# Optimization experiments

Measured on AMD Instinct MI355X. Metric: run time of the kernel, lower is better.

Reference implementation:

```python
import jax, jax.numpy as jnp
import numpy as np

T = 2048      # sequence length (single unbatched sequence)
V = 32000     # vocab
D = 1024      # d_model
E = 16        # number of experts (one structural group)
TOPK = 2      # router top-k
CAP = 256     # per-expert capacity (T*TOPK/E)
DFF = 2048    # expert MLP hidden
NHOPS = 2     # number of routing hops
EPS = 1e-5    # RMSNorm eps


def setup_inputs() -> dict:
    key = jax.random.key(0)
    ks = jax.random.split(key, 6)
    ids = jax.random.randint(ks[0], (T,), 0, V)
    embed_W = jax.random.normal(ks[1], (V, D), jnp.float32) * 0.02
    ln_scale = jnp.ones((D,), jnp.float32)
    router_W = jax.random.normal(ks[2], (NHOPS, D, E), jnp.float32) * (D ** -0.5)
    expert_W1 = jax.random.normal(ks[3], (NHOPS, E, D, DFF), jnp.float32) * (D ** -0.5)
    expert_W2 = jax.random.normal(ks[4], (NHOPS, E, DFF, D), jnp.float32) * (DFF ** -0.5)
    return dict(ids=ids, embed_W=embed_W, ln_scale=ln_scale,
                router_W=router_W, expert_W1=expert_W1, expert_W2=expert_W2)


def _hop(h, Wr, W1, W2):
    # Router: clean logits -> mixing probs (softmax) + hard top-k selection mask.
    logits = h @ Wr                                   # (T, E)
    probs = jax.nn.softmax(logits, axis=-1)           # (T, E)
    _, top = jax.lax.top_k(logits, TOPK)              # (T, TOPK)
    mask = jnp.zeros((T, E), bool).at[jnp.arange(T)[:, None], top].set(True)

    # _capacity_select: rank tokens per expert by clean logits, keep top CAP.
    m = mask.T                                        # (E, T)
    g = jnp.where(m, logits.T, -jnp.inf)              # (E, T)
    _, top_idx = jax.lax.top_k(g, CAP)                # (E, C)
    slot = jnp.zeros((E, CAP, T), h.dtype)
    slot = slot.at[jnp.arange(E)[:, None], jnp.arange(CAP)[None, :], top_idx].set(1.0)
    slot = slot * m[:, None, :].astype(h.dtype)       # zero slots filled from -inf
    kept = slot.sum(1) > 0                            # (E, T)

    # One-hot einsum gather of token states into expert slot buffers.
    xin = jnp.einsum('ect,td->ecd', slot, h)          # (E, C, D)

    # Stable sort slots by original token position (active slots first).
    active = slot.sum(-1) > 0                         # (E, C)
    pos = jnp.where(active, top_idx, T + 1)
    order = jnp.argsort(pos, axis=1, stable=True)     # (E, C)
    xin = jnp.take_along_axis(xin, order[:, :, None], axis=1)
    slot = jnp.take_along_axis(slot, order[:, :, None], axis=1)

    # Grouped (stacked/vmapped) expert execution: GELU MLP per expert.
    h1 = jax.nn.gelu(jnp.einsum('ecd,edf->ecf', xin, W1))
    expert_out = jnp.einsum('ecf,efd->ecd', h1, W2)   # (E, C, D)

    # Combine (Eq. 3): h_{s+1} = h_s + sum_e rho_e (M_e(h) - h)
    cw = jnp.where(kept.T, probs, 0.0)                # (T, E)
    rho = cw.sum(axis=1, keepdims=True)               # (T, 1)
    combine = jnp.einsum('ecd,ect,et->td', expert_out, slot, cw.T)
    return h + combine - rho * h


def reference(ids, embed_W, ln_scale, router_W, expert_W1, expert_W2):
    h = embed_W[ids]                                  # (T, D) embedding lookup
    for i in range(NHOPS):
        h = _hop(h, router_W[i], expert_W1[i], expert_W2[i])
    # RMSNorm + tied unembedding
    h = h * jax.lax.rsqrt(jnp.mean(h * h, axis=-1, keepdims=True) + EPS) * ln_scale
    return h @ embed_W.T                              # (T, V)
```

## Files before the change

### kernel.cpp

```cpp
#include <hip/hip_runtime.h>
#include <stdint.h>

#define T_ 2048
#define V_ 32000
#define D_ 1024
#define E_ 16
#define CAP_ 256
#define DFF_ 2048

typedef unsigned short u16;
typedef unsigned int u32;
typedef __bf16 bf16x8 __attribute__((ext_vector_type(8)));
typedef float f32x4 __attribute__((ext_vector_type(4)));

__device__ __forceinline__ u16 f2bf(float f){
  u32 u = __float_as_uint(f);
  u32 r = u + 0x7FFFu + ((u >> 16) & 1u);
  return (u16)(r >> 16);
}
__device__ __forceinline__ float bf2f(u16 s){ return __uint_as_float(((u32)s) << 16); }

__device__ __forceinline__ void gl_lds16(const void* g, void* l){
  __builtin_amdgcn_global_load_lds((const __attribute__((address_space(1))) void*)g,
                                   (__attribute__((address_space(3))) void*)l, 16, 0, 0);
}
__device__ __forceinline__ f32x4 mfma16(bf16x8 a, bf16x8 b, f32x4 c){
  return __builtin_amdgcn_mfma_f32_16x16x32_bf16(a, b, c, 0, 0, 0);
}
__device__ __forceinline__ float gelu_tanh(float x){
  float u = 0.7978845608028654f * (x + 0.044715f * x * x * x);
  return 0.5f * x * (1.0f + tanhf(u));
}

__global__ __launch_bounds__(256) void k_embed(const int* __restrict__ ids,
    const float* __restrict__ W, float* __restrict__ h){
  int t = blockIdx.x;
  int d = threadIdx.x * 4;
  *(float4*)(h + (size_t)t*D_ + d) = *(const float4*)(W + (size_t)ids[t]*D_ + d);
}

__global__ __launch_bounds__(256) void k_cvtw(const float* __restrict__ W, u16* __restrict__ Wb){
  size_t i = ((size_t)blockIdx.x*256 + threadIdx.x)*8;
  float4 a = *(const float4*)(W + i);
  float4 b = *(const float4*)(W + i + 4);
  union { u16 s[8]; uint4 v; } p;
  p.s[0]=f2bf(a.x); p.s[1]=f2bf(a.y); p.s[2]=f2bf(a.z); p.s[3]=f2bf(a.w);
  p.s[4]=f2bf(b.x); p.s[5]=f2bf(b.y); p.s[6]=f2bf(b.z); p.s[7]=f2bf(b.w);
  *(uint4*)(Wb + i) = p.v;
}

__global__ __launch_bounds__(256) void k_router(const float* __restrict__ h,
    const float* __restrict__ Wr, float* __restrict__ logits,
    unsigned char* __restrict__ mask, int* __restrict__ top2, float* __restrict__ p2){
  int w = threadIdx.x >> 6, l = threadIdx.x & 63;
  int t = blockIdx.x*4 + w;
  float acc[E_];
  #pragma unroll
  for (int e=0;e<E_;++e) acc[e]=0.f;
  const float* hrow = h + (size_t)t*D_;
  #pragma unroll
  for (int i=0;i<16;++i){
    int d = l + i*64;
    float hv = hrow[d];
    const float4* wr = (const float4*)(Wr + d*E_);
    float4 w0=wr[0], w1=wr[1], w2=wr[2], w3=wr[3];
    acc[0]+=hv*w0.x; acc[1]+=hv*w0.y; acc[2]+=hv*w0.z; acc[3]+=hv*w0.w;
    acc[4]+=hv*w1.x; acc[5]+=hv*w1.y; acc[6]+=hv*w1.z; acc[7]+=hv*w1.w;
    acc[8]+=hv*w2.x; acc[9]+=hv*w2.y; acc[10]+=hv*w2.z; acc[11]+=hv*w2.w;
    acc[12]+=hv*w3.x; acc[13]+=hv*w3.y; acc[14]+=hv*w3.z; acc[15]+=hv*w3.w;
  }
  #pragma unroll
  for (int off=32; off; off>>=1){
    #pragma unroll
    for (int e=0;e<E_;++e) acc[e] += __shfl_xor(acc[e], off, 64);
  }
  float mx = acc[0];
  #pragma unroll
  for (int e=1;e<E_;++e) mx = fmaxf(mx, acc[e]);
  float p[E_], s = 0.f;
  #pragma unroll
  for (int e=0;e<E_;++e){ p[e] = expf(acc[e]-mx); s += p[e]; }
  int i1 = 0; float v1 = acc[0];
  #pragma unroll
  for (int e=1;e<E_;++e) if (acc[e] > v1){ v1 = acc[e]; i1 = e; }
  int i2 = (i1==0)?1:0; float v2 = acc[i2];
  #pragma unroll
  for (int e=0;e<E_;++e) if (e!=i1 && e!=i2 && acc[e] > v2){ v2 = acc[e]; i2 = e; }
  if (l < E_){
    logits[t*E_+l] = acc[l];
    mask[t*E_+l] = (l==i1 || l==i2) ? 1 : 0;
  }
  if (l == 0){
    float inv = 1.f/s;
    top2[t*2] = i1; top2[t*2+1] = i2;
    p2[t*2] = p[i1]*inv; p2[t*2+1] = p[i2]*inv;
  }
}

__global__ __launch_bounds__(256) void k_init_etok(int* __restrict__ etok){
  etok[blockIdx.x*256 + threadIdx.x] = -1;
}

__global__ __launch_bounds__(256) void k_capacity(const float* __restrict__ logits,
    const unsigned char* __restrict__ mask, const int* __restrict__ top2,
    int* __restrict__ kept, int* __restrict__ etok){
  int w = threadIdx.x >> 6, l = threadIdx.x & 63;
  int wid = blockIdx.x*4 + w;
  int t = wid >> 1, k = wid & 1;
  int e = top2[t*2+k];
  float my = logits[t*E_+e];
  int cnt = 0;
  for (int t2 = l; t2 < T_; t2 += 64){
    if (mask[t2*E_+e]){
      float lg = logits[t2*E_+e];
      if (lg > my || (lg == my && t2 < t)) cnt++;
    }
  }
  #pragma unroll
  for (int off=32; off; off>>=1) cnt += __shfl_xor(cnt, off, 64);
  if (l == 0){
    if (cnt < CAP_){ kept[t*2+k] = cnt; etok[e*CAP_+cnt] = t; }
    else kept[t*2+k] = -1;
  }
}

__global__ __launch_bounds__(256) void k_gather(const float* __restrict__ h,
    const int* __restrict__ etok, u16* __restrict__ xhi, u16* __restrict__ xlo){
  int rc = blockIdx.x;
  int tok = etok[rc];
  int d = threadIdx.x * 4;
  float4 v = make_float4(0.f,0.f,0.f,0.f);
  if (tok >= 0) v = *(const float4*)(h + (size_t)tok*D_ + d);
  union { u16 s[4]; uint2 u; } hi, lo;
  hi.s[0]=f2bf(v.x); lo.s[0]=f2bf(v.x - bf2f(hi.s[0]));
  hi.s[1]=f2bf(v.y); lo.s[1]=f2bf(v.y - bf2f(hi.s[1]));
  hi.s[2]=f2bf(v.z); lo.s[2]=f2bf(v.z - bf2f(hi.s[2]));
  hi.s[3]=f2bf(v.w); lo.s[3]=f2bf(v.w - bf2f(hi.s[3]));
  *(uint2*)(xhi + (size_t)rc*D_ + d) = hi.u;
  *(uint2*)(xlo + (size_t)rc*D_ + d) = lo.u;
}

template<bool SPLIT, bool GELU>
__global__ __launch_bounds__(256, 2) void k_gemm_expert(
    const u16* __restrict__ Ahi, const u16* __restrict__ Alo,
    const float* __restrict__ Bw,
    u16* __restrict__ Ohi, u16* __restrict__ Olo, float* __restrict__ Of,
    int N, int K, int ntiles){
  constexpr int NB = SPLIT ? 2 : 1;
  __shared__ __align__(16) u16 As[NB*128*32];
  __shared__ __align__(16) u16 Bs[NB*128*40];
  u16* AsLo = As + 128*32;
  u16* BsLo = Bs + 128*40;
  int chunk = gridDim.x >> 3;
  int bid = blockIdx.x;
  int swz = (bid & 7)*chunk + (bid >> 3);
  int e = swz / (2*ntiles);
  int rem = swz - e*2*ntiles;
  int nt = rem >> 1, mt = rem & 1;
  int m0 = mt*128, n0 = nt*128;
  int tid = threadIdx.x;
  int l = tid & 63;
  int wr = tid >> 7, wc = (tid >> 6) & 1;
  int lr = l & 15, lq = l >> 4;
  int kb = tid >> 5, nb = tid & 31;
  const u16* Ah = Ahi + (size_t)e*256*K;
  const u16* Al = SPLIT ? (Alo + (size_t)e*256*K) : (const u16*)nullptr;
  const float* Bb = Bw + (size_t)e*K*N;
  f32x4 acc[4][4];
  #pragma unroll
  for (int i=0;i<4;++i)
    #pragma unroll
    for (int j=0;j<4;++j)
      #pragma unroll
      for (int c=0;c<4;++c) acc[i][j][c] = 0.f;

  float4 pb0, pb1, pb2, pb3;
  {
    const float* bs = Bb + (size_t)(kb*4)*N + n0 + nb*4;
    pb0 = *(const float4*)bs;
    pb1 = *(const float4*)(bs + N);
    pb2 = *(const float4*)(bs + 2*N);
    pb3 = *(const float4*)(bs + 3*N);
  }

  for (int k0 = 0; k0 < K; k0 += 32){
    __syncthreads();
    #pragma unroll
    for (int r=0;r<2;++r){
      int o = r*4096 + tid*16;
      int row = o >> 6;
      int c = (o >> 4) & 3;
      int cs = c ^ ((row >> 1) & 3);
      gl_lds16(Ah + (size_t)(m0+row)*K + k0 + cs*8, (char*)As + o);
      if constexpr (SPLIT)
        gl_lds16(Al + (size_t)(m0+row)*K + k0 + cs*8, (char*)AsLo + o);
    }
    {
      float cv[4][4] = {{pb0.x,pb1.x,pb2.x,pb3.x},{pb0.y,pb1.y,pb2.y,pb3.y},
                        {pb0.z,pb1.z,pb2.z,pb3.z},{pb0.w,pb1.w,pb2.w,pb3.w}};
      #pragma unroll
      for (int j=0;j<4;++j){
        int n = nb*4 + j;
        union { u16 s[4]; uint2 u; } hi, lo;
        #pragma unroll
        for (int i=0;i<4;++i){
          hi.s[i] = f2bf(cv[j][i]);
          if constexpr (SPLIT) lo.s[i] = f2bf(cv[j][i] - bf2f(hi.s[i]));
        }
        *(uint2*)((char*)Bs + n*80 + kb*8) = hi.u;
        if constexpr (SPLIT) *(uint2*)((char*)BsLo + n*80 + kb*8) = lo.u;
      }
    }
    if (k0 + 32 < K){
      const float* bs = Bb + (size_t)(k0 + 32 + kb*4)*N + n0 + nb*4;
      pb0 = *(const float4*)bs;
      pb1 = *(const float4*)(bs + N);
      pb2 = *(const float4*)(bs + 2*N);
      pb3 = *(const float4*)(bs + 3*N);
    }
    __syncthreads();
    bf16x8 ah[4], al[4], bh[4], bl[4];
    #pragma unroll
    for (int mi=0;mi<4;++mi){
      int row = wr*64 + mi*16 + lr;
      int q = lq ^ ((row >> 1) & 3);
      int o = row*64 + q*16;
      ah[mi] = *(const bf16x8*)((const char*)As + o);
      if constexpr (SPLIT) al[mi] = *(const bf16x8*)((const char*)AsLo + o);
    }
    #pragma unroll
    for (int ni=0;ni<4;++ni){
      int o = (wc*64 + ni*16 + lr)*80 + lq*16;
      bh[ni] = *(const bf16x8*)((const char*)Bs + o);
      if constexpr (SPLIT) bl[ni] = *(const bf16x8*)((const char*)BsLo + o);
    }
    #pragma unroll
    for (int mi=0;mi<4;++mi)
      #pragma unroll
      for (int ni=0;ni<4;++ni){
        acc[mi][ni] = mfma16(ah[mi], bh[ni], acc[mi][ni]);
        if constexpr (SPLIT){
          acc[mi][ni] = mfma16(al[mi], bh[ni], acc[mi][ni]);
          acc[mi][ni] = mfma16(ah[mi], bl[ni], acc[mi][ni]);
        }
      }
  }
  #pragma unroll
  for (int mi=0;mi<4;++mi)
    #pragma unroll
    for (int ni=0;ni<4;++ni)
      #pragma unroll
      for (int j=0;j<4;++j){
        int row = m0 + wr*64 + mi*16 + lq*4 + j;
        int col = n0 + wc*64 + ni*16 + lr;
        float x = acc[mi][ni][j];
        size_t idx = ((size_t)e*256 + row)*N + col;
        if constexpr (GELU){
          float y = gelu_tanh(x);
          u16 hv = f2bf(y);
          Ohi[idx] = hv;
          if constexpr (SPLIT) Olo[idx] = f2bf(y - bf2f(hv));
        } else {
          Of[idx] = x;
        }
      }
}

__global__ __launch_bounds__(256) void k_combine(float* __restrict__ h,
    const float* __restrict__ Y2, const int* __restrict__ top2,
    const float* __restrict__ p2, const int* __restrict__ kept){
  int t = blockIdx.x;
  int e0 = top2[t*2], e1 = top2[t*2+1];
  int r0 = kept[t*2], r1 = kept[t*2+1];
  float w0 = (r0 >= 0) ? p2[t*2]   : 0.f;
  float w1 = (r1 >= 0) ? p2[t*2+1] : 0.f;
  float om = 1.f - w0 - w1;
  int d = threadIdx.x * 4;
  float4 v = *(const float4*)(h + (size_t)t*D_ + d);
  float ox = v.x*om, oy = v.y*om, oz = v.z*om, ow = v.w*om;
  if (r0 >= 0){
    float4 y = *(const float4*)(Y2 + ((size_t)e0*CAP_ + r0)*D_ + d);
    ox += w0*y.x; oy += w0*y.y; oz += w0*y.z; ow += w0*y.w;
  }
  if (r1 >= 0){
    float4 y = *(const float4*)(Y2 + ((size_t)e1*CAP_ + r1)*D_ + d);
    ox += w1*y.x; oy += w1*y.y; oz += w1*y.z; ow += w1*y.w;
  }
  *(float4*)(h + (size_t)t*D_ + d) = make_float4(ox, oy, oz, ow);
}

__global__ __launch_bounds__(256) void k_rmsnorm(const float* __restrict__ h,
    const float* __restrict__ g, u16* __restrict__ hn){
  int t = blockIdx.x;
  int d = threadIdx.x * 4;
  int w = threadIdx.x >> 6, l = threadIdx.x & 63;
  __shared__ float red[4];
  float4 v = *(const float4*)(h + (size_t)t*D_ + d);
  float ss = v.x*v.x + v.y*v.y + v.z*v.z + v.w*v.w;
  #pragma unroll
  for (int off=32; off; off>>=1) ss += __shfl_xor(ss, off, 64);
  if (l == 0) red[w] = ss;
  __syncthreads();
  float tot = red[0] + red[1] + red[2] + red[3];
  float sc = rsqrtf(tot * (1.f/D_) + 1e-5f);
  float4 gs = *(const float4*)(g + d);
  union { u16 s[4]; uint2 u; } o;
  o.s[0] = f2bf(v.x*sc*gs.x); o.s[1] = f2bf(v.y*sc*gs.y);
  o.s[2] = f2bf(v.z*sc*gs.z); o.s[3] = f2bf(v.w*sc*gs.w);
  *(uint2*)(hn + (size_t)t*D_ + d) = o.u;
}

#define SLOT_ 16384
__global__ __launch_bounds__(512, 2) void k_gemm_final(const u16* __restrict__ A,
    const u16* __restrict__ B, float* __restrict__ C){
  __shared__ __align__(16) char lds[131072];
  char* ldsA = lds;
  char* ldsB = lds + 65536;
  int bid = blockIdx.x;
  int wgid = (bid & 7) * 125 + (bid >> 3);
  int m0 = (wgid & 7) << 8;
  int n0 = (wgid >> 3) << 8;
  int tid = threadIdx.x;
  int lane = tid & 63;
  int w = tid >> 6;
  int wm = w >> 2, wn = w & 3;
  int lr = lane & 15, lq = lane >> 4;

  f32x4 acc[8][4];
  #pragma unroll
  for (int i=0;i<8;++i)
    #pragma unroll
    for (int j=0;j<4;++j)
      #pragma unroll
      for (int c=0;c<4;++c) acc[i][j][c] = 0.f;

  int j_0 = w*2, j_1 = w*2 + 1;
  int rp0 = j_0*8 + (lane>>3), rp1 = j_1*8 + (lane>>3);
  int c80 = (lane&7) ^ (rp0&7), c81 = (lane&7) ^ (rp1&7);
  int rA0 = rp0*2 + (c80>>2), rA1 = rp1*2 + (c81>>2);
  int cc0 = (c80&3)*8,        cc1 = (c81&3)*8;
  const u16* sA0 = A + (size_t)(m0+rA0)*D_ + cc0;
  const u16* sA1 = A + (size_t)(m0+rA1)*D_ + cc1;
  const u16* sB0 = B + (size_t)(n0+rA0)*D_ + cc0;
  const u16* sB1 = B + (size_t)(n0+rA1)*D_ + cc1;
  int d0 = j_0*1024 + lane*16, d1 = j_1*1024 + lane*16;

  int aoff[8], boff[4];
  #pragma unroll
  for (int mi=0;mi<8;++mi){
    int r = wm*128 + mi*16 + lr;
    int rp = r >> 1;
    int c8 = ((r&1)<<2) | lq;
    aoff[mi] = rp*128 + ((c8 ^ (rp&7))<<4);
  }
  #pragma unroll
  for (int ni=0;ni<4;++ni){
    int r = wn*64 + ni*16 + lr;
    int rp = r >> 1;
    int c8 = ((r&1)<<2) | lq;
    boff[ni] = rp*128 + ((c8 ^ (rp&7))<<4);
  }

  #define STAGE_(sbase) do { \
    gl_lds16(sA0, ldsA + (sbase) + d0); gl_lds16(sB0, ldsB + (sbase) + d0); \
    gl_lds16(sA1, ldsA + (sbase) + d1); gl_lds16(sB1, ldsB + (sbase) + d1); \
    sA0 += 32; sA1 += 32; sB0 += 32; sB1 += 32; } while(0)

  STAGE_(0); STAGE_(SLOT_); STAGE_(2*SLOT_);

  for (int kh = 0; kh < 32; ++kh){
    if (kh < 30)       asm volatile("s_waitcnt vmcnt(8)" ::: "memory");
    else if (kh == 30) asm volatile("s_waitcnt vmcnt(4)" ::: "memory");
    else               asm volatile("s_waitcnt vmcnt(0)" ::: "memory");
    __builtin_amdgcn_sched_barrier(0);
    __builtin_amdgcn_s_barrier();
    __builtin_amdgcn_sched_barrier(0);
    if (kh <= 28) STAGE_(((kh+3)&3)*SLOT_);
    int sb = (kh & 3) * SLOT_;
    const char* pA = ldsA + sb;
    const char* pB = ldsB + sb;
    bf16x8 b[4];
    #pragma unroll
    for (int ni=0;ni<4;++ni) b[ni] = *(const bf16x8*)(pB + boff[ni]);
    __builtin_amdgcn_s_setprio(1);
    #pragma unroll
    for (int mi=0;mi<8;++mi){
      bf16x8 a = *(const bf16x8*)(pA + aoff[mi]);
      #pragma unroll
      for (int ni=0;ni<4;++ni)
        acc[mi][ni] = mfma16(a, b[ni], acc[mi][ni]);
    }
    __builtin_amdgcn_s_setprio(0);
  }
  #undef STAGE_

  #pragma unroll
  for (int mi=0;mi<8;++mi)
    #pragma unroll
    for (int ni=0;ni<4;++ni)
      #pragma unroll
      for (int j=0;j<4;++j){
        int row = m0 + wm*128 + mi*16 + lq*4 + j;
        int col = n0 + wn*64 + ni*16 + lr;
        C[(size_t)row * V_ + col] = acc[mi][ni][j];
      }
}

extern "C" void kernel_launch(void* const* d_in, const int* in_sizes, int n_in,
                              void* d_out, int out_size, void* d_ws, size_t ws_size,
                              hipStream_t stream){
  const int*   ids  = (const int*)d_in[0];
  const float* embW = (const float*)d_in[1];
  const float* lns  = (const float*)d_in[2];
  const float* WrA  = (const float*)d_in[3];
  const float* W1A  = (const float*)d_in[4];
  const float* W2A  = (const float*)d_in[5];
  float* out = (float*)d_out;
  char* ws = (char*)d_ws;
  const size_t MB = 1u << 20;

  float* h      = (float*)(ws);
  float* logits = (float*)(ws + 8*MB);
  unsigned char* mask = (unsigned char*)(ws + 8*MB + 131072);
  int*   top2v  = (int*)(ws + 8*MB + 131072 + 32768);
  float* p2     = (float*)(ws + 8*MB + 131072 + 32768 + 16384);
  int*   kept   = (int*)(ws + 8*MB + 131072 + 32768 + 32768);
  int*   etok   = (int*)(ws + 8*MB + 131072 + 32768 + 49152);
  u16*   xhi  = (u16*)(ws + 9*MB);
  u16*   xlo  = (u16*)(ws + 17*MB);
  float* y2   = (float*)(ws + 9*MB);
  u16*   y1hi = (u16*)(ws + 25*MB);
  u16*   y1lo = (u16*)(ws + 41*MB);
  u16*   hn   = (u16*)(ws + 57*MB);
  u16*   ebf  = (u16*)(ws + 61*MB);

  k_embed<<<T_, 256, 0, stream>>>(ids, embW, h);
  k_cvtw<<<(V_*D_)/(256*8), 256, 0, stream>>>(embW, ebf);

  for (int hop = 0; hop < 2; ++hop){
    const float* Wr = WrA + (size_t)hop*D_*E_;
    const float* W1 = W1A + (size_t)hop*E_*D_*DFF_;
    const float* W2 = W2A + (size_t)hop*E_*DFF_*D_;
    k_router<<<T_/4, 256, 0, stream>>>(h, Wr, logits, mask, top2v, p2);
    k_init_etok<<<E_*CAP_/256, 256, 0, stream>>>(etok);
    k_capacity<<<T_*2/4, 256, 0, stream>>>(logits, mask, top2v, kept, etok);
    k_gather<<<E_*CAP_, 256, 0, stream>>>(h, etok, xhi, xlo);
    if (hop == 0){
      k_gemm_expert<true , true ><<<E_*2*(DFF_/128), 256, 0, stream>>>(
          xhi, xlo, W1, y1hi, y1lo, nullptr, DFF_, D_, DFF_/128);
      k_gemm_expert<true , false><<<E_*2*(D_/128), 256, 0, stream>>>(
          y1hi, y1lo, W2, nullptr, nullptr, y2, D_, DFF_, D_/128);
    } else {
      k_gemm_expert<false, true ><<<E_*2*(DFF_/128), 256, 0, stream>>>(
          xhi, nullptr, W1, y1hi, nullptr, nullptr, DFF_, D_, DFF_/128);
      k_gemm_expert<false, false><<<E_*2*(D_/128), 256, 0, stream>>>(
          y1hi, nullptr, W2, nullptr, nullptr, y2, D_, DFF_, D_/128);
    }
    k_combine<<<T_, 256, 0, stream>>>(h, y2, top2v, p2, kept);
  }

  k_rmsnorm<<<T_, 256, 0, stream>>>(h, lns, hn);
  k_gemm_final<<<(T_/256)*(V_/256), 512, 0, stream>>>(hn, ebf, out);
}
```

Measured before the change: 676.9 us.

## Fuse embed/init into router, rmsnorm into combine, double-buffer final GEMM fragments

```diff
diff --git a/kernel.cpp b/kernel.cpp
--- a/kernel.cpp
+++ b/kernel.cpp
@@ -30,13 +30,6 @@
 __device__ __forceinline__ float gelu_tanh(float x){
   float u = 0.7978845608028654f * (x + 0.044715f * x * x * x);
   return 0.5f * x * (1.0f + tanhf(u));
-}
-
-__global__ __launch_bounds__(256) void k_embed(const int* __restrict__ ids,
-    const float* __restrict__ W, float* __restrict__ h){
-  int t = blockIdx.x;
-  int d = threadIdx.x * 4;
-  *(float4*)(h + (size_t)t*D_ + d) = *(const float4*)(W + (size_t)ids[t]*D_ + d);
 }
 
 __global__ __launch_bounds__(256) void k_cvtw(const float* __restrict__ W, u16* __restrict__ Wb){
@@ -49,19 +42,23 @@
   *(uint4*)(Wb + i) = p.v;
 }
 
-__global__ __launch_bounds__(256) void k_router(const float* __restrict__ h,
+template<bool EMB>
+__global__ __launch_bounds__(256) void k_router(float* __restrict__ h,
     const float* __restrict__ Wr, float* __restrict__ logits,
-    unsigned char* __restrict__ mask, int* __restrict__ top2, float* __restrict__ p2){
+    unsigned char* __restrict__ mask, int* __restrict__ top2, float* __restrict__ p2,
+    const int* __restrict__ ids, const float* __restrict__ embW, int* __restrict__ etok){
+  if (blockIdx.x < (E_*CAP_)/256) etok[blockIdx.x*256 + threadIdx.x] = -1;
   int w = threadIdx.x >> 6, l = threadIdx.x & 63;
   int t = blockIdx.x*4 + w;
   float acc[E_];
   #pragma unroll
   for (int e=0;e<E_;++e) acc[e]=0.f;
-  const float* hrow = h + (size_t)t*D_;
+  const float* hrow = EMB ? (embW + (size_t)ids[t]*D_) : (h + (size_t)t*D_);
   #pragma unroll
   for (int i=0;i<16;++i){
     int d = l + i*64;
     float hv = hrow[d];
+    if (EMB) h[(size_t)t*D_ + d] = hv;
     const float4* wr = (const float4*)(Wr + d*E_);
     float4 w0=wr[0], w1=wr[1], w2=wr[2], w3=wr[3];
     acc[0]+=hv*w0.x; acc[1]+=hv*w0.y; acc[2]+=hv*w0.z; acc[3]+=hv*w0.w;
@@ -95,10 +92,6 @@
     top2[t*2] = i1; top2[t*2+1] = i2;
     p2[t*2] = p[i1]*inv; p2[t*2+1] = p[i2]*inv;
   }
-}
-
-__global__ __launch_bounds__(256) void k_init_etok(int* __restrict__ etok){
-  etok[blockIdx.x*256 + threadIdx.x] = -1;
 }
 
 __global__ __launch_bounds__(256) void k_capacity(const float* __restrict__ logits,
@@ -266,9 +259,11 @@
       }
 }
 
+template<bool FINAL>
 __global__ __launch_bounds__(256) void k_combine(float* __restrict__ h,
     const float* __restrict__ Y2, const int* __restrict__ top2,
-    const float* __restrict__ p2, const int* __restrict__ kept){
+    const float* __restrict__ p2, const int* __restrict__ kept,
+    const float* __restrict__ g, u16* __restrict__ hn){
   int t = blockIdx.x;
   int e0 = top2[t*2], e1 = top2[t*2+1];
   int r0 = kept[t*2], r1 = kept[t*2+1];
@@ -286,28 +281,24 @@
     float4 y = *(const float4*)(Y2 + ((size_t)e1*CAP_ + r1)*D_ + d);
     ox += w1*y.x; oy += w1*y.y; oz += w1*y.z; ow += w1*y.w;
   }
-  *(float4*)(h + (size_t)t*D_ + d) = make_float4(ox, oy, oz, ow);
-}
-
-__global__ __launch_bounds__(256) void k_rmsnorm(const float* __restrict__ h,
-    const float* __restrict__ g, u16* __restrict__ hn){
-  int t = blockIdx.x;
-  int d = threadIdx.x * 4;
-  int w = threadIdx.x >> 6, l = threadIdx.x & 63;
-  __shared__ float red[4];
-  float4 v = *(const float4*)(h + (size_t)t*D_ + d);
-  float ss = v.x*v.x + v.y*v.y + v.z*v.z + v.w*v.w;
-  #pragma unroll
-  for (int off=32; off; off>>=1) ss += __shfl_xor(ss, off, 64);
-  if (l == 0) red[w] = ss;
-  __syncthreads();
-  float tot = red[0] + red[1] + red[2] + red[3];
-  float sc = rsqrtf(tot * (1.f/D_) + 1e-5f);
-  float4 gs = *(const float4*)(g + d);
-  union { u16 s[4]; uint2 u; } o;
-  o.s[0] = f2bf(v.x*sc*gs.x); o.s[1] = f2bf(v.y*sc*gs.y);
-  o.s[2] = f2bf(v.z*sc*gs.z); o.s[3] = f2bf(v.w*sc*gs.w);
-  *(uint2*)(hn + (size_t)t*D_ + d) = o.u;
+  if constexpr (!FINAL){
+    *(float4*)(h + (size_t)t*D_ + d) = make_float4(ox, oy, oz, ow);
+  } else {
+    int w = threadIdx.x >> 6, l = threadIdx.x & 63;
+    __shared__ float red[4];
+    float ss = ox*ox + oy*oy + oz*oz + ow*ow;
+    #pragma unroll
+    for (int off=32; off; off>>=1) ss += __shfl_xor(ss, off, 64);
+    if (l == 0) red[w] = ss;
+    __syncthreads();
+    float tot = red[0] + red[1] + red[2] + red[3];
+    float sc = rsqrtf(tot * (1.f/D_) + 1e-5f);
+    float4 gs = *(const float4*)(g + d);
+    union { u16 s[4]; uint2 u; } o;
+    o.s[0] = f2bf(ox*sc*gs.x); o.s[1] = f2bf(oy*sc*gs.y);
+    o.s[2] = f2bf(oz*sc*gs.z); o.s[3] = f2bf(ow*sc*gs.w);
+    *(uint2*)(hn + (size_t)t*D_ + d) = o.u;
+  }
 }
 
 #define SLOT_ 16384
@@ -366,32 +357,47 @@
     gl_lds16(sA1, ldsA + (sbase) + d1); gl_lds16(sB1, ldsB + (sbase) + d1); \
     sA0 += 32; sA1 += 32; sB0 += 32; sB1 += 32; } while(0)
 
+  bf16x8 aF0[8], bF0[4], aF1[8], bF1[4];
+
   STAGE_(0); STAGE_(SLOT_); STAGE_(2*SLOT_);
-
-  for (int kh = 0; kh < 32; ++kh){
-    if (kh < 30)       asm volatile("s_waitcnt vmcnt(8)" ::: "memory");
-    else if (kh == 30) asm volatile("s_waitcnt vmcnt(4)" ::: "memory");
-    else               asm volatile("s_waitcnt vmcnt(0)" ::: "memory");
-    __builtin_amdgcn_sched_barrier(0);
-    __builtin_amdgcn_s_barrier();
-    __builtin_amdgcn_sched_barrier(0);
-    if (kh <= 28) STAGE_(((kh+3)&3)*SLOT_);
-    int sb = (kh & 3) * SLOT_;
-    const char* pA = ldsA + sb;
-    const char* pB = ldsB + sb;
-    bf16x8 b[4];
-    #pragma unroll
-    for (int ni=0;ni<4;++ni) b[ni] = *(const bf16x8*)(pB + boff[ni]);
-    __builtin_amdgcn_s_setprio(1);
-    #pragma unroll
-    for (int mi=0;mi<8;++mi){
-      bf16x8 a = *(const bf16x8*)(pA + aoff[mi]);
-      #pragma unroll
-      for (int ni=0;ni<4;++ni)
-        acc[mi][ni] = mfma16(a, b[ni], acc[mi][ni]);
-    }
-    __builtin_amdgcn_s_setprio(0);
-  }
+  asm volatile("s_waitcnt vmcnt(8)" ::: "memory");
+  __builtin_amdgcn_s_barrier();
+  {
+    const char* pA_ = ldsA; const char* pB_ = ldsB;
+    #pragma unroll
+    for (int ni=0;ni<4;++ni) bF0[ni] = *(const bf16x8*)(pB_ + boff[ni]);
+    #pragma unroll
+    for (int mi=0;mi<8;++mi) aF0[mi] = *(const bf16x8*)(pA_ + aoff[mi]);
+  }
+
+  #define PHASE_(kh, FAc, FBc, FAn, FBn) do { \
+    if ((kh) <= 28) STAGE_((((kh)+3)&3)*SLOT_); \
+    if ((kh) <= 28)      asm volatile("s_waitcnt vmcnt(8)" ::: "memory"); \
+    else if ((kh) == 29) asm volatile("s_waitcnt vmcnt(4)" ::: "memory"); \
+    else if ((kh) == 30) asm volatile("s_waitcnt vmcnt(0)" ::: "memory"); \
+    asm volatile("s_waitcnt lgkmcnt(0)" ::: "memory"); \
+    __builtin_amdgcn_sched_barrier(0); \
+    __builtin_amdgcn_s_barrier(); \
+    __builtin_amdgcn_sched_barrier(0); \
+    if ((kh) < 31){ \
+      int sb_ = (((kh)+1)&3)*SLOT_; \
+      const char* pA_ = ldsA + sb_; const char* pB_ = ldsB + sb_; \
+      _Pragma("unroll") for (int ni=0;ni<4;++ni) FBn[ni] = *(const bf16x8*)(pB_ + boff[ni]); \
+      _Pragma("unroll") for (int mi=0;mi<8;++mi) FAn[mi] = *(const bf16x8*)(pA_ + aoff[mi]); \
+    } \
+    __builtin_amdgcn_s_setprio(1); \
+    _Pragma("unroll") for (int mi=0;mi<8;++mi){ \
+      _Pragma("unroll") for (int ni=0;ni<4;++ni) \
+        acc[mi][ni] = mfma16(FAc[mi], FBc[ni], acc[mi][ni]); \
+    } \
+    __builtin_amdgcn_s_setprio(0); \
+  } while(0)
+
+  for (int kh2 = 0; kh2 < 32; kh2 += 2){
+    PHASE_(kh2,     aF0, bF0, aF1, bF1);
+    PHASE_(kh2 + 1, aF1, bF1, aF0, bF0);
+  }
+  #undef PHASE_
   #undef STAGE_
 
   #pragma unroll
@@ -434,15 +440,16 @@
   u16*   hn   = (u16*)(ws + 57*MB);
   u16*   ebf  = (u16*)(ws + 61*MB);
 
-  k_embed<<<T_, 256, 0, stream>>>(ids, embW, h);
   k_cvtw<<<(V_*D_)/(256*8), 256, 0, stream>>>(embW, ebf);
 
   for (int hop = 0; hop < 2; ++hop){
     const float* Wr = WrA + (size_t)hop*D_*E_;
     const float* W1 = W1A + (size_t)hop*E_*D_*DFF_;
     const float* W2 = W2A + (size_t)hop*E_*DFF_*D_;
-    k_router<<<T_/4, 256, 0, stream>>>(h, Wr, logits, mask, top2v, p2);
-    k_init_etok<<<E_*CAP_/256, 256, 0, stream>>>(etok);
+    if (hop == 0)
+      k_router<true ><<<T_/4, 256, 0, stream>>>(h, Wr, logits, mask, top2v, p2, ids, embW, etok);
+    else
+      k_router<false><<<T_/4, 256, 0, stream>>>(h, Wr, logits, mask, top2v, p2, ids, embW, etok);
     k_capacity<<<T_*2/4, 256, 0, stream>>>(logits, mask, top2v, kept, etok);
     k_gather<<<E_*CAP_, 256, 0, stream>>>(h, etok, xhi, xlo);
     if (hop == 0){
@@ -450,15 +457,15 @@
           xhi, xlo, W1, y1hi, y1lo, nullptr, DFF_, D_, DFF_/128);
       k_gemm_expert<true , false><<<E_*2*(D_/128), 256, 0, stream>>>(
           y1hi, y1lo, W2, nullptr, nullptr, y2, D_, DFF_, D_/128);
+      k_combine<false><<<T_, 256, 0, stream>>>(h, y2, top2v, p2, kept, lns, hn);
     } else {
       k_gemm_expert<false, true ><<<E_*2*(DFF_/128), 256, 0, stream>>>(
           xhi, nullptr, W1, y1hi, nullptr, nullptr, DFF_, D_, DFF_/128);
       k_gemm_expert<false, false><<<E_*2*(D_/128), 256, 0, stream>>>(
           y1hi, nullptr, W2, nullptr, nullptr, y2, D_, DFF_, D_/128);
-    }
-    k_combine<<<T_, 256, 0, stream>>>(h, y2, top2v, p2, kept);
-  }
-
-  k_rmsnorm<<<T_, 256, 0, stream>>>(h, lns, hn);
+      k_combine<true ><<<T_, 256, 0, stream>>>(h, y2, top2v, p2, kept, lns, hn);
+    }
+  }
+
   k_gemm_final<<<(T_/256)*(V_/256), 512, 0, stream>>>(hn, ebf, out);
 }
```

After: 714.7 us. 1.06x slower.
